# Performance work log

Hardware: AMD Instinct MI355X
Metric: run time of the kernel (lower is better)

Reference implementation:

```python
import jax, jax.numpy as jnp
import numpy as np

N_CAM = 6; C = 256; K = 100; GK = 200; NUM_CLASSES = 10; PROB_BIN = 64
SHAPES = [(72, 128), (36, 64), (18, 32)]
H_PAD, W_PAD = 576.0, 1024.0


def _make_anchors(shapes, grid_size=0.05, eps=0.01):
    parts = []
    for lvl, (h, w) in enumerate(shapes):
        gy, gx = jnp.meshgrid(jnp.arange(h, dtype=jnp.float32), jnp.arange(w, dtype=jnp.float32), indexing='ij')
        xy = (jnp.stack([gx, gy], -1) + 0.5) / jnp.array([w, h], jnp.float32)
        wh = jnp.full_like(xy, grid_size * 2.0 ** lvl)
        parts.append(jnp.concatenate([xy, wh], -1).reshape(-1, 4))
    a = jnp.concatenate(parts, 0)[None]  # [1, L, 4]
    valid = jnp.all((a > eps) & (a < 1 - eps), -1, keepdims=True)
    a = jnp.where(valid, jnp.log(a / (1 - a)), jnp.inf)
    return a, valid


def _layernorm(x, g, b, eps=1e-5):
    m = jnp.mean(x, -1, keepdims=True)
    v = jnp.var(x, -1, keepdims=True)
    return (x - m) * jax.lax.rsqrt(v + eps) * g + b


def _center2lidar(c2d, depths, intr, ext_inv):
    # c2d: [NK,2], depths: [NK,D], intr/ext_inv: [NK,4,4]
    fx = jnp.clip(intr[:, 0, 0], 1e-6)[:, None]
    fy = jnp.clip(intr[:, 1, 1], 1e-6)[:, None]
    cx = intr[:, 0, 2][:, None]; cy = intr[:, 1, 2][:, None]
    X = (c2d[:, 0:1] - cx) / fx * depths
    Y = (c2d[:, 1:2] - cy) / fy * depths
    pts = jnp.stack([X, Y, depths, jnp.ones_like(depths)], -1)  # [NK, D, 4]
    return jnp.einsum('ndk,njk->ndj', pts, ext_inv)[..., :3]


def setup_inputs():
    key = jax.random.key(0)
    ks = iter(jax.random.split(key, 48))
    def feat(shape):
        return jax.random.normal(next(ks), shape, dtype=jnp.float32)
    def w(shape):
        return (jax.random.normal(next(ks), shape) * 0.02).astype(jnp.float32)
    inp = {}
    for i, (h, wdt) in enumerate(SHAPES):
        inp[f'feat{i}'] = feat((N_CAM, C, h, wdt))
    rng = np.random.default_rng(0)
    Km = np.tile(np.eye(4, dtype=np.float32), (N_CAM, 1, 1))
    Km[:, 0, 0] = 500.0 + 10.0 * rng.standard_normal(N_CAM)
    Km[:, 1, 1] = 500.0 + 10.0 * rng.standard_normal(N_CAM)
    Km[:, 0, 2] = 512.0; Km[:, 1, 2] = 288.0
    E = np.tile(np.eye(4, dtype=np.float32), (N_CAM, 1, 1))
    for i in range(N_CAM):
        th = 2.0 * np.pi * i / N_CAM
        E[i, :3, :3] = np.array([[np.cos(th), -np.sin(th), 0.0], [np.sin(th), np.cos(th), 0.0], [0.0, 0.0, 1.0]], np.float32)
        E[i, :3, 3] = rng.standard_normal(3).astype(np.float32)
    inp['intrinsics'] = jnp.asarray(Km)[None]
    inp['extrinsics'] = jnp.asarray(E)[None]
    inp['extrinsics_inv'] = jnp.asarray(np.linalg.inv(E).astype(np.float32))[None]
    inp['w_proj0'] = w((C, C)); inp['w_proj1'] = w((C, C)); inp['w_proj2'] = w((C, C))
    inp['w_enc'] = w((C, C)); inp['b_enc'] = jnp.zeros((C,), jnp.float32)
    inp['ln_g'] = jnp.ones((C,), jnp.float32); inp['ln_b'] = jnp.zeros((C,), jnp.float32)
    inp['w_cls'] = w((C, NUM_CLASSES)); inp['b_cls'] = jnp.zeros((NUM_CLASSES,), jnp.float32)
    inp['w_bb1'] = w((C, C)); inp['b_bb1'] = jnp.zeros((C,), jnp.float32)
    inp['w_bb2'] = w((C, C)); inp['b_bb2'] = jnp.zeros((C,), jnp.float32)
    inp['w_bb3'] = w((C, 4)); inp['b_bb3'] = jnp.zeros((4,), jnp.float32)
    inp['depth_bins'] = jnp.linspace(1.0, 60.0, PROB_BIN, dtype=jnp.float32)
    inp['w_d1'] = w((C + 16, C)); inp['b_d1'] = jnp.zeros((C,), jnp.float32)
    inp['w_d2'] = w((C, PROB_BIN)); inp['b_d2'] = jnp.zeros((PROB_BIN,), jnp.float32)
    inp['w_m1'] = w((14, C)); inp['b_m1'] = jnp.zeros((C,), jnp.float32)
    inp['w_mg'] = w((C, C)); inp['b_mg'] = jnp.ones((C,), jnp.float32)
    inp['w_mb'] = w((C, C)); inp['b_mb'] = jnp.zeros((C,), jnp.float32)
    return inp


def reference(feat0, feat1, feat2, intrinsics, extrinsics, extrinsics_inv,
              w_proj0, w_proj1, w_proj2, w_enc, b_enc, ln_g, ln_b,
              w_cls, b_cls, w_bb1, b_bb1, w_bb2, b_bb2, w_bb3, b_bb3,
              depth_bins, w_d1, b_d1, w_d2, b_d2,
              w_m1, b_m1, w_mg, b_mg, w_mb, b_mb):
    intr = intrinsics[0]; ext = extrinsics[0]; ext_inv = extrinsics_inv[0]
    feats = [feat0, feat1, feat2]
    projs = [w_proj0, w_proj1, w_proj2]
    # flatten to [N_cam, HW, C] and apply 1x1 input projection
    tok = [jnp.einsum('nchw,cd->nhwd', f, wp).reshape(N_CAM, -1, C) for f, wp in zip(feats, projs)]
    memory = jnp.concatenate(tok, axis=1)  # [N_cam, L, C]
    anchors, valid = _make_anchors(SHAPES)
    out_mem = _layernorm((memory * valid.astype(memory.dtype)) @ w_enc + b_enc, ln_g, ln_b)
    enc_cls = out_mem @ w_cls + b_cls
    h = jax.nn.relu(out_mem @ w_bb1 + b_bb1)
    h = jax.nn.relu(h @ w_bb2 + b_bb2)
    enc_bbox = h @ w_bb3 + b_bb3 + anchors
    topk_scores, topk_ind = jax.lax.top_k(jnp.max(enc_cls, -1), K)  # [N_cam, K]
    query_feats = jnp.take_along_axis(out_mem, topk_ind[..., None], axis=1)  # [N_cam, K, C]
    ref_boxes = jax.nn.sigmoid(jnp.take_along_axis(enc_bbox, topk_ind[..., None], axis=1))  # [N_cam, K, 4]
    NK = N_CAM * K
    intr_q = jnp.broadcast_to(intr[:, None], (N_CAM, K, 4, 4)).reshape(NK, 4, 4)
    ext_inv_q = jnp.broadcast_to(ext_inv[:, None], (N_CAM, K, 4, 4)).reshape(NK, 4, 4)
    qf_flat = jax.lax.stop_gradient(query_feats).reshape(NK, C)
    depth_in = jnp.concatenate([qf_flat, intr_q.reshape(NK, 16) * 0.01], -1)
    dl = jax.nn.relu(depth_in @ w_d1 + b_d1) @ w_d2 + b_d2
    dl = jnp.nan_to_num(dl, nan=0.0, posinf=1e4, neginf=-1e4)
    depth_prob = jax.nn.softmax(dl.astype(jnp.float32), -1)  # [NK, D]
    c2d = jnp.stack([ref_boxes[..., 0].reshape(-1) * W_PAD, ref_boxes[..., 1].reshape(-1) * H_PAD], -1)
    depths = jnp.broadcast_to(depth_bins[None], (NK, PROB_BIN))
    center = _center2lidar(c2d, depths, intr_q, ext_inv_q)  # [NK, D, 3]
    dyn_query = jnp.concatenate([center, depth_prob[..., None]], -1)  # [NK, D, 4]
    _, gidx = jax.lax.top_k(topk_scores.reshape(-1), GK)
    dyn_query = dyn_query[gidx]
    qf_out = qf_flat[gidx]
    # MLN spatial alignment over raw encoder levels 0..1
    intr_s = intr / 1000.0
    mln_in = jnp.concatenate([intr_s[:, 0, 0:1], intr_s[:, 1, 1:2], ext[:, :3, :].reshape(N_CAM, 12)], -1)[:, None]  # [N,1,14]
    ff = jnp.concatenate([feat0.reshape(N_CAM, C, -1).transpose(0, 2, 1),
                          feat1.reshape(N_CAM, C, -1).transpose(0, 2, 1)], 1)  # [N, L_img, C]
    hm = jax.nn.relu(mln_in @ w_m1 + b_m1)
    gamma = hm @ w_mg + b_mg
    beta = hm @ w_mb + b_mb
    feat_flatten = ff * gamma + beta
    spatial_flatten = jnp.array([[s[0], s[1]] for s in SHAPES[:2]], jnp.int32)
    lidar2img = jnp.einsum('nij,njk->nik', intr, ext)[None]
    return (feat_flatten, spatial_flatten, lidar2img, dyn_query[None], qf_out[None])
```

## Files before the change

### kernel.cpp

```cpp
#include <hip/hip_runtime.h>
#include <math.h>

#define DEVI __device__ __forceinline__

constexpr int CAMS = 6;
constexpr int CH   = 256;
constexpr int LTOT = 12096;
constexpr int TPC  = 189;
constexpr int LIMG = 11520;

constexpr size_t WS_OM = 0;
constexpr size_t WS_SC = WS_OM + (size_t)CAMS*LTOT*CH;
constexpr size_t WS_TI = WS_SC + (size_t)CAMS*LTOT;
constexpr size_t WS_TS = WS_TI + 768;
constexpr size_t WS_DA = WS_TS + 768;
constexpr size_t WS_GI = WS_DA + (size_t)600*256;
constexpr size_t WS_GS = WS_GI + 256;
constexpr size_t WS_GA = WS_GS + 256;
constexpr size_t WS_BE = WS_GA + 1536;
constexpr size_t WS_AI = WS_BE + 1536;
constexpr size_t WS_AS = WS_AI + 3712;

constexpr size_t O_FF  = 0;
constexpr size_t O_SP  = (size_t)CAMS*LIMG*CH;
constexpr size_t O_L2I = O_SP + 4;
constexpr size_t O_DQ  = O_L2I + 96;
constexpr size_t O_QF  = O_DQ + (size_t)200*64*4;

DEVI float anchor_comp(int l, int j) {
    int W, wsh, ll; float Wf, Hf;
    if (l < 9216)      { W=128; wsh=7; Wf=128.f; Hf=72.f; ll=l; }
    else if (l < 11520){ W=64;  wsh=6; Wf=64.f;  Hf=36.f; ll=l-9216; }
    else               { W=32;  wsh=5; Wf=32.f;  Hf=18.f; ll=l-11520; }
    int y = ll >> wsh, x = ll & (W-1);
    float px = (x + 0.5f) / Wf;
    float py = (y + 0.5f) / Hf;
    bool valid = (px > 0.01f) && (px < 0.99f) && (py > 0.01f) && (py < 0.99f);
    if (!valid) return INFINITY;
    float p = (j == 0) ? px : py;
    return logf(p / (1.f - p));
}

__global__ __launch_bounds__(256, 3)
void k_proj(const float* __restrict__ f0, const float* __restrict__ f1, const float* __restrict__ f2,
            const float* __restrict__ wp0, const float* __restrict__ wp1, const float* __restrict__ wp2,
            float* __restrict__ Mout)
{
    __shared__ __align__(16) float lds[2*2048 + 2*512];
    float* wbufs = lds;
    float* abufs = lds + 4096;

    const int bx = blockIdx.x;
    const int n  = bx / TPC;
    const int l0 = (bx % TPC) * 64;
    const float* feat; const float* wp;
    int HW, lloc, W, wsh; float Wf, Hf;
    if (l0 < 9216)      { feat=f0; wp=wp0; HW=9216; lloc=l0;       W=128; wsh=7; Wf=128.f; Hf=72.f; }
    else if (l0 < 11520){ feat=f1; wp=wp1; HW=2304; lloc=l0-9216;  W=64;  wsh=6; Wf=64.f;  Hf=36.f; }
    else                { feat=f2; wp=wp2; HW=576;  lloc=l0-11520; W=32;  wsh=5; Wf=32.f;  Hf=18.f; }
    const float* featn = feat + (size_t)n*CH*HW;

    const int tid  = threadIdx.x;
    const int rg   = tid >> 5;
    const int cg   = tid & 31;
    const int sc_  = tid >> 5;
    const int sg   = tid & 31;
    const int arow = tid >> 4;
    const int ag   = tid & 15;

    float4 wreg0, wreg1;
    float4 areg;

    auto loadW = [&](int ck) {
        const float* p = wp + (size_t)(ck*8 + sc_)*256 + sg*8;
        wreg0 = *reinterpret_cast<const float4*>(p);
        wreg1 = *reinterpret_cast<const float4*>(p + 4);
    };
    auto writeW = [&](int b) {
        float* d = wbufs + b*2048 + sc_*256;
        *reinterpret_cast<float4*>(d + sg*4)       = wreg0;
        *reinterpret_cast<float4*>(d + 128 + sg*4) = wreg1;
    };
    auto loadA = [&](int ck) {
        if (tid < 128)
            areg = *reinterpret_cast<const float4*>(featn + (size_t)(ck*8 + arow)*HW + lloc + ag*4);
    };
    auto writeA = [&](int b) {
        if (tid < 128)
            *reinterpret_cast<float4*>(abufs + b*512 + arow*64 + ag*4) = areg;
    };

    float acc[8][8];
    #pragma unroll
    for (int r=0;r<8;++r)
        #pragma unroll
        for (int j=0;j<8;++j) acc[r][j] = 0.f;

    loadW(0); loadA(0);
    writeW(0); writeA(0);
    __syncthreads();
    int buf = 0;
    for (int k = 0; k < 32; ++k) {
        if (k < 31) { loadW(k+1); loadA(k+1); }
        const float* wb = wbufs + buf*2048;
        const float* ab = abufs + buf*512;
        #pragma unroll 2
        for (int c = 0; c < 8; ++c) {
            float4 a0 = *reinterpret_cast<const float4*>(ab + c*64 + rg*8);
            float4 a1 = *reinterpret_cast<const float4*>(ab + c*64 + rg*8 + 4);
            float4 w0 = *reinterpret_cast<const float4*>(wb + c*256 + cg*4);
            float4 w1 = *reinterpret_cast<const float4*>(wb + c*256 + 128 + cg*4);
            float av[8] = {a0.x,a0.y,a0.z,a0.w, a1.x,a1.y,a1.z,a1.w};
            float wv[8] = {w0.x,w0.y,w0.z,w0.w, w1.x,w1.y,w1.z,w1.w};
            #pragma unroll
            for (int r=0;r<8;++r)
                #pragma unroll
                for (int j=0;j<8;++j)
                    acc[r][j] = fmaf(av[r], wv[j], acc[r][j]);
        }
        if (k < 31) { writeW(buf^1); writeA(buf^1); }
        __syncthreads();
        buf ^= 1;
    }

    #pragma unroll
    for (int r=0;r<8;++r) {
        int ll = lloc + rg*8 + r;
        int y = ll >> wsh, x = ll & (W-1);
        float px = (x + 0.5f) / Wf;
        float py = (y + 0.5f) / Hf;
        bool valid = (px > 0.01f) && (px < 0.99f) && (py > 0.01f) && (py < 0.99f);
        float m = valid ? 1.f : 0.f;
        float* dst = Mout + ((size_t)n*LTOT + l0 + rg*8 + r)*CH + cg*8;
        *reinterpret_cast<float4*>(dst)   = make_float4(acc[r][0]*m,acc[r][1]*m,acc[r][2]*m,acc[r][3]*m);
        *reinterpret_cast<float4*>(dst+4) = make_float4(acc[r][4]*m,acc[r][5]*m,acc[r][6]*m,acc[r][7]*m);
    }
}

__global__ __launch_bounds__(256, 3)
void k_enc(float* __restrict__ M,
           const float* __restrict__ w_enc, const float* __restrict__ b_enc,
           const float* __restrict__ ln_g, const float* __restrict__ ln_b,
           const float* __restrict__ w_cls, const float* __restrict__ b_cls,
           float* __restrict__ scores)
{
    __shared__ __align__(16) float lds[2*2048 + 2*512];
    float* wbufs = lds;
    float* abufs = lds + 4096;

    const int bx = blockIdx.x;
    const int n  = bx / TPC;
    const int l0 = (bx % TPC) * 64;

    const int tid  = threadIdx.x;
    const int rg   = tid >> 5;
    const int cg   = tid & 31;
    const int sc_  = tid >> 5;
    const int sg   = tid & 31;
    const int tok  = tid & 63;
    const int cq   = (tid >> 6) & 1;

    float4 wreg0, wreg1;
    float4 mreg;

    auto loadW = [&](int ck) {
        const float* p = w_enc + (size_t)(ck*8 + sc_)*256 + sg*8;
        wreg0 = *reinterpret_cast<const float4*>(p);
        wreg1 = *reinterpret_cast<const float4*>(p + 4);
    };
    auto writeW = [&](int b) {
        float* d = wbufs + b*2048 + sc_*256;
        *reinterpret_cast<float4*>(d + sg*4)       = wreg0;
        *reinterpret_cast<float4*>(d + 128 + sg*4) = wreg1;
    };
    auto loadA = [&](int ck) {
        if (tid < 128)
            mreg = *reinterpret_cast<const float4*>(M + ((size_t)n*LTOT + l0 + tok)*CH + ck*8 + cq*4);
    };
    auto writeA = [&](int b) {
        if (tid < 128) {
            float* d = abufs + b*512 + tok;
            d[(cq*4+0)*64] = mreg.x;
            d[(cq*4+1)*64] = mreg.y;
            d[(cq*4+2)*64] = mreg.z;
            d[(cq*4+3)*64] = mreg.w;
        }
    };

    float acc[8][8];
    #pragma unroll
    for (int r=0;r<8;++r)
        #pragma unroll
        for (int j=0;j<8;++j) acc[r][j] = 0.f;

    loadW(0); loadA(0);
    writeW(0); writeA(0);
    __syncthreads();
    int buf = 0;
    for (int k = 0; k < 32; ++k) {
        if (k < 31) { loadW(k+1); loadA(k+1); }
        const float* wb = wbufs + buf*2048;
        const float* ab = abufs + buf*512;
        #pragma unroll 2
        for (int c = 0; c < 8; ++c) {
            float4 a0 = *reinterpret_cast<const float4*>(ab + c*64 + rg*8);
            float4 a1 = *reinterpret_cast<const float4*>(ab + c*64 + rg*8 + 4);
            float4 w0 = *reinterpret_cast<const float4*>(wb + c*256 + cg*4);
            float4 w1 = *reinterpret_cast<const float4*>(wb + c*256 + 128 + cg*4);
            float av[8] = {a0.x,a0.y,a0.z,a0.w, a1.x,a1.y,a1.z,a1.w};
            float wv[8] = {w0.x,w0.y,w0.z,w0.w, w1.x,w1.y,w1.z,w1.w};
            #pragma unroll
            for (int r=0;r<8;++r)
                #pragma unroll
                for (int j=0;j<8;++j)
                    acc[r][j] = fmaf(av[r], wv[j], acc[r][j]);
        }
        if (k < 31) { writeW(buf^1); writeA(buf^1); }
        __syncthreads();
        buf ^= 1;
    }

    {
        float4 be0 = *reinterpret_cast<const float4*>(b_enc + cg*8);
        float4 be1 = *reinterpret_cast<const float4*>(b_enc + cg*8 + 4);
        float4 g0  = *reinterpret_cast<const float4*>(ln_g  + cg*8);
        float4 g1  = *reinterpret_cast<const float4*>(ln_g  + cg*8 + 4);
        float4 bb0 = *reinterpret_cast<const float4*>(ln_b  + cg*8);
        float4 bb1 = *reinterpret_cast<const float4*>(ln_b  + cg*8 + 4);
        float bev[8] = {be0.x,be0.y,be0.z,be0.w, be1.x,be1.y,be1.z,be1.w};
        float gv[8]  = {g0.x,g0.y,g0.z,g0.w, g1.x,g1.y,g1.z,g1.w};
        float bv[8]  = {bb0.x,bb0.y,bb0.z,bb0.w, bb1.x,bb1.y,bb1.z,bb1.w};
        #pragma unroll
        for (int r=0;r<8;++r) {
            float s = 0.f;
            #pragma unroll
            for (int j=0;j<8;++j) { acc[r][j] += bev[j]; s += acc[r][j]; }
            s += __shfl_xor(s,1); s += __shfl_xor(s,2); s += __shfl_xor(s,4);
            s += __shfl_xor(s,8); s += __shfl_xor(s,16);
            float mean = s * (1.f/256.f);
            float vs = 0.f;
            #pragma unroll
            for (int j=0;j<8;++j) { float d = acc[r][j]-mean; vs = fmaf(d,d,vs); }
            vs += __shfl_xor(vs,1); vs += __shfl_xor(vs,2); vs += __shfl_xor(vs,4);
            vs += __shfl_xor(vs,8); vs += __shfl_xor(vs,16);
            float rs = 1.f / sqrtf(vs*(1.f/256.f) + 1e-5f);
            #pragma unroll
            for (int j=0;j<8;++j) acc[r][j] = (acc[r][j]-mean)*rs*gv[j] + bv[j];
        }
    }

    #pragma unroll
    for (int r=0;r<8;++r) {
        float* dst = M + ((size_t)n*LTOT + l0 + rg*8 + r)*CH + cg*8;
        *reinterpret_cast<float4*>(dst)   = make_float4(acc[r][0],acc[r][1],acc[r][2],acc[r][3]);
        *reinterpret_cast<float4*>(dst+4) = make_float4(acc[r][4],acc[r][5],acc[r][6],acc[r][7]);
    }

    {
        float bcl[10];
        #pragma unroll
        for (int c=0;c<10;++c) bcl[c] = b_cls[c];
        #pragma unroll
        for (int r=0;r<8;++r) {
            float p[10];
            #pragma unroll
            for (int c=0;c<10;++c) p[c] = 0.f;
            #pragma unroll
            for (int i=0;i<8;++i) {
                const float* wc = w_cls + (cg*8+i)*10;
                float a = acc[r][i];
                #pragma unroll
                for (int c=0;c<10;c+=2) {
                    float2 w2 = *reinterpret_cast<const float2*>(wc + c);
                    p[c]   = fmaf(a, w2.x, p[c]);
                    p[c+1] = fmaf(a, w2.y, p[c+1]);
                }
            }
            #pragma unroll
            for (int c=0;c<10;++c) {
                p[c] += __shfl_xor(p[c],1); p[c] += __shfl_xor(p[c],2);
                p[c] += __shfl_xor(p[c],4); p[c] += __shfl_xor(p[c],8);
                p[c] += __shfl_xor(p[c],16);
            }
            if (cg == 0) {
                float mx = -INFINITY;
                #pragma unroll
                for (int c=0;c<10;++c) mx = fmaxf(mx, p[c] + bcl[c]);
                scores[(size_t)n*LTOT + l0 + rg*8 + r] = mx;
            }
        }
    }
}

typedef unsigned long long u64;

DEVI u64 pack_key(float s, unsigned idx) {
    unsigned u = __float_as_uint(s);
    u = (u & 0x80000000u) ? ~u : (u | 0x80000000u);
    return ((u64)u << 32) | (unsigned)(~idx);
}
DEVI float key_score(u64 k) {
    unsigned u = (unsigned)(k >> 32);
    u = (u & 0x80000000u) ? (u ^ 0x80000000u) : ~u;
    return __uint_as_float(u);
}
DEVI int key_idx(u64 k) { return (int)(~(unsigned)k); }

template<int N>
DEVI void bitonic_desc(u64* s, int tid) {
    for (int size = 2; size <= N; size <<= 1) {
        for (int stride = size >> 1; stride > 0; stride >>= 1) {
            __syncthreads();
            #pragma unroll 2
            for (int t = tid; t < N/2; t += 256) {
                int lo = ((t & ~(stride-1)) << 1) | (t & (stride-1));
                int hi = lo + stride;
                bool desc = ((lo & size) == 0);
                u64 a = s[lo], b = s[hi];
                if ((a < b) == desc) { s[lo] = b; s[hi] = a; }
            }
        }
    }
    __syncthreads();
}

__global__ __launch_bounds__(256)
void k_sortA(const float* __restrict__ scores, int* __restrict__ outi, float* __restrict__ outs)
{
    __shared__ u64 s[2048];
    const int b = blockIdx.x, tid = threadIdx.x;
    const int cam = b / 6, seg = b % 6;
    const float* v = scores + (size_t)cam*LTOT + seg*2016;
    for (int i = tid; i < 2048; i += 256)
        s[i] = (i < 2016) ? pack_key(v[i], seg*2016 + i) : 0ull;
    bitonic_desc<2048>(s, tid);
    if (tid < 100) {
        u64 k = s[tid];
        outi[b*100 + tid] = key_idx(k);
        outs[b*100 + tid] = key_score(k);
    }
}

__global__ __launch_bounds__(256)
void k_sortB(const int* __restrict__ ai, const float* __restrict__ as,
             int* __restrict__ ti, float* __restrict__ ts)
{
    __shared__ u64 s[1024];
    const int cam = blockIdx.x, tid = threadIdx.x;
    for (int i = tid; i < 1024; i += 256)
        s[i] = (i < 600) ? pack_key(as[cam*600 + i], (unsigned)ai[cam*600 + i]) : 0ull;
    bitonic_desc<1024>(s, tid);
    if (tid < 100) {
        u64 k = s[tid];
        ti[cam*100 + tid] = key_idx(k);
        ts[cam*100 + tid] = key_score(k);
    }
}

__global__ __launch_bounds__(256)
void k_sortC(const float* __restrict__ ts, int* __restrict__ gi)
{
    __shared__ u64 s[1024];
    const int tid = threadIdx.x;
    for (int i = tid; i < 1024; i += 256)
        s[i] = (i < 600) ? pack_key(ts[i], (unsigned)i) : 0ull;
    bitonic_desc<1024>(s, tid);
    if (tid < 200) gi[tid] = key_idx(s[tid]);
}

__global__ __launch_bounds__(256)
void k_query(const float* __restrict__ out_mem, const int* __restrict__ topk_ind,
             const float* __restrict__ intr, const float* __restrict__ ext_inv,
             const float* __restrict__ w_bb1, const float* __restrict__ b_bb1,
             const float* __restrict__ w_bb2, const float* __restrict__ b_bb2,
             const float* __restrict__ w_bb3, const float* __restrict__ b_bb3,
             const float* __restrict__ depth_bins,
             const float* __restrict__ w_d1, const float* __restrict__ b_d1,
             const float* __restrict__ w_d2, const float* __restrict__ b_d2,
             float* __restrict__ dyn_all)
{
    __shared__ float sq[272];
    __shared__ float sh[256];
    __shared__ float sh2[256];
    __shared__ float sbb[2];
    const int nk = blockIdx.x;
    const int n = nk / 100;
    const int tid = threadIdx.x;
    const int l = topk_ind[nk];
    sq[tid] = out_mem[((size_t)n*LTOT + l)*CH + tid];
    if (tid < 16) sq[256+tid] = intr[n*16+tid] * 0.01f;
    __syncthreads();
    float s1 = b_bb1[tid];
    for (int c=0;c<256;++c) s1 = fmaf(sq[c], w_bb1[c*256+tid], s1);
    sh[tid] = fmaxf(s1, 0.f);
    __syncthreads();
    float s2 = b_bb2[tid];
    for (int c=0;c<256;++c) s2 = fmaf(sh[c], w_bb2[c*256+tid], s2);
    sh2[tid] = fmaxf(s2, 0.f);
    __syncthreads();
    {
        int j = tid >> 6, c0 = tid & 63;
        if (j < 2) {
            float p = 0.f;
            #pragma unroll
            for (int t=0;t<4;++t) { int c = c0 + t*64; p = fmaf(sh2[c], w_bb3[c*4+j], p); }
            #pragma unroll
            for (int m=1;m<64;m<<=1) p += __shfl_xor(p, m);
            if (c0 == 0) sbb[j] = p + b_bb3[j] + anchor_comp(l, j);
        }
    }
    float t1 = b_d1[tid];
    for (int c=0;c<272;++c) t1 = fmaf(sq[c], w_d1[c*256+tid], t1);
    sh[tid] = fmaxf(t1, 0.f);
    __syncthreads();
    if (tid < 64) {
        float dl = b_d2[tid];
        for (int c=0;c<256;++c) dl = fmaf(sh[c], w_d2[c*64+tid], dl);
        if (isnan(dl)) dl = 0.f;
        if (isinf(dl)) dl = (dl > 0.f) ? 1e4f : -1e4f;
        float mx = dl;
        #pragma unroll
        for (int m=1;m<64;m<<=1) mx = fmaxf(mx, __shfl_xor(mx, m));
        float e = expf(dl - mx);
        float sum = e;
        #pragma unroll
        for (int m=1;m<64;m<<=1) sum += __shfl_xor(sum, m);
        float dp = e / sum;
        float fx = fmaxf(intr[n*16+0], 1e-6f);
        float fy = fmaxf(intr[n*16+5], 1e-6f);
        float cx = intr[n*16+2], cy = intr[n*16+6];
        float sx = 1.f/(1.f+expf(-sbb[0]));
        float sy = 1.f/(1.f+expf(-sbb[1]));
        float c2dx = sx * 1024.f, c2dy = sy * 576.f;
        float dep = depth_bins[tid];
        float X = (c2dx - cx)/fx*dep;
        float Y = (c2dy - cy)/fy*dep;
        const float* EI = ext_inv + n*16;
        float c0v = EI[0]*X + EI[1]*Y + EI[2]*dep + EI[3];
        float c1v = EI[4]*X + EI[5]*Y + EI[6]*dep + EI[7];
        float c2v = EI[8]*X + EI[9]*Y + EI[10]*dep + EI[11];
        float4 o = make_float4(c0v, c1v, c2v, dp);
        *reinterpret_cast<float4*>(dyn_all + ((size_t)nk*64 + tid)*4) = o;
    }
}

__global__ __launch_bounds__(256)
void k_gather(const float* __restrict__ dyn_all, const int* __restrict__ gidx,
              const int* __restrict__ topk_ind, const float* __restrict__ out_mem,
              float* __restrict__ out)
{
    int g = blockIdx.x, tid = threadIdx.x;
    int src = gidx[g];
    out[O_DQ + (size_t)g*256 + tid] = dyn_all[(size_t)src*256 + tid];
    int n = src/100; int l = topk_ind[src];
    out[O_QF + (size_t)g*256 + tid] = out_mem[((size_t)n*LTOT + l)*CH + tid];
}

__global__ __launch_bounds__(256)
void k_mln(const float* __restrict__ intr, const float* __restrict__ ext,
           const float* __restrict__ w_m1, const float* __restrict__ b_m1,
           const float* __restrict__ w_mg, const float* __restrict__ b_mg,
           const float* __restrict__ w_mb, const float* __restrict__ b_mb,
           float* __restrict__ gamma, float* __restrict__ beta)
{
    __shared__ float hm[256];
    int tid = threadIdx.x;
    for (int n=0;n<CAMS;++n) {
        float m[14];
        m[0] = intr[n*16+0] / 1000.0f;
        m[1] = intr[n*16+5] / 1000.0f;
        #pragma unroll
        for (int j=0;j<12;++j) m[2+j] = ext[n*16+j];
        float h = b_m1[tid];
        #pragma unroll
        for (int k=0;k<14;++k) h = fmaf(m[k], w_m1[k*256+tid], h);
        hm[tid] = fmaxf(h, 0.f);
        __syncthreads();
        float g = b_mg[tid], bt = b_mb[tid];
        for (int c=0;c<256;++c) {
            float hv = hm[c];
            g  = fmaf(hv, w_mg[c*256+tid], g);
            bt = fmaf(hv, w_mb[c*256+tid], bt);
        }
        gamma[n*256+tid] = g;
        beta[n*256+tid]  = bt;
        __syncthreads();
    }
}

__global__ __launch_bounds__(256)
void k_flatten(const float* __restrict__ f0, const float* __restrict__ f1,
               const float* __restrict__ gamma, const float* __restrict__ beta,
               float* __restrict__ out)
{
    __shared__ float t[64][65];
    int b = blockIdx.x;
    int lt = b % 180, ct = (b/180) & 3, n = b / 720;
    int l0 = lt*64, c0 = ct*64;
    const float* f; int HW, lb;
    if (l0 < 9216) { f=f0; HW=9216; lb=l0; } else { f=f1; HW=2304; lb=l0-9216; }
    int tid = threadIdx.x;
    int cl = tid >> 4, lw = (tid & 15)*4;
    #pragma unroll
    for (int rep=0;rep<4;++rep) {
        int cc = cl + rep*16;
        float4 v = *reinterpret_cast<const float4*>(f + ((size_t)n*CH + c0+cc)*HW + lb + lw);
        t[cc][lw+0]=v.x; t[cc][lw+1]=v.y; t[cc][lw+2]=v.z; t[cc][lw+3]=v.w;
    }
    __syncthreads();
    int ll = tid >> 4, cw = (tid & 15)*4;
    float4 gv = *reinterpret_cast<const float4*>(gamma + n*256 + c0 + cw);
    float4 bv = *reinterpret_cast<const float4*>(beta  + n*256 + c0 + cw);
    #pragma unroll
    for (int rep=0;rep<4;++rep) {
        int l = ll + rep*16;
        float4 o;
        o.x = fmaf(t[cw+0][l], gv.x, bv.x);
        o.y = fmaf(t[cw+1][l], gv.y, bv.y);
        o.z = fmaf(t[cw+2][l], gv.z, bv.z);
        o.w = fmaf(t[cw+3][l], gv.w, bv.w);
        *reinterpret_cast<float4*>(out + ((size_t)n*LIMG + l0 + l)*CH + c0 + cw) = o;
    }
}

__global__ void k_small(const float* __restrict__ intr, const float* __restrict__ ext,
                        float* __restrict__ out)
{
    int tid = threadIdx.x;
    if (tid < 4) {
        const float sp[4] = {72.f, 128.f, 36.f, 64.f};
        out[O_SP + tid] = sp[tid];
    }
    if (tid < 96) {
        int n = tid >> 4, i = (tid >> 2) & 3, k = tid & 3;
        float s = 0.f;
        #pragma unroll
        for (int j=0;j<4;++j) s = fmaf(intr[n*16 + i*4 + j], ext[n*16 + j*4 + k], s);
        out[O_L2I + tid] = s;
    }
}

extern "C" void kernel_launch(void* const* d_in, const int* in_sizes, int n_in,
                              void* d_out, int out_size, void* d_ws, size_t ws_size,
                              hipStream_t stream) {
    const float* f0      = (const float*)d_in[0];
    const float* f1      = (const float*)d_in[1];
    const float* f2      = (const float*)d_in[2];
    const float* intr    = (const float*)d_in[3];
    const float* ext     = (const float*)d_in[4];
    const float* ext_inv = (const float*)d_in[5];
    const float* wp0     = (const float*)d_in[6];
    const float* wp1     = (const float*)d_in[7];
    const float* wp2     = (const float*)d_in[8];
    const float* w_enc   = (const float*)d_in[9];
    const float* b_enc   = (const float*)d_in[10];
    const float* ln_g    = (const float*)d_in[11];
    const float* ln_b    = (const float*)d_in[12];
    const float* w_cls   = (const float*)d_in[13];
    const float* b_cls   = (const float*)d_in[14];
    const float* w_bb1   = (const float*)d_in[15];
    const float* b_bb1   = (const float*)d_in[16];
    const float* w_bb2   = (const float*)d_in[17];
    const float* b_bb2   = (const float*)d_in[18];
    const float* w_bb3   = (const float*)d_in[19];
    const float* b_bb3   = (const float*)d_in[20];
    const float* dbins   = (const float*)d_in[21];
    const float* w_d1    = (const float*)d_in[22];
    const float* b_d1    = (const float*)d_in[23];
    const float* w_d2    = (const float*)d_in[24];
    const float* b_d2    = (const float*)d_in[25];
    const float* w_m1    = (const float*)d_in[26];
    const float* b_m1    = (const float*)d_in[27];
    const float* w_mg    = (const float*)d_in[28];
    const float* b_mg    = (const float*)d_in[29];
    const float* w_mb    = (const float*)d_in[30];
    const float* b_mb    = (const float*)d_in[31];

    float* ws  = (float*)d_ws;
    float* out = (float*)d_out;
    float* om  = ws + WS_OM;
    float* sc  = ws + WS_SC;
    int*   ti  = (int*)(ws + WS_TI);
    float* ts  = ws + WS_TS;
    float* da  = ws + WS_DA;
    int*   gi  = (int*)(ws + WS_GI);
    float* ga  = ws + WS_GA;
    float* be  = ws + WS_BE;
    int*   ai  = (int*)(ws + WS_AI);
    float* as  = ws + WS_AS;

    k_proj<<<CAMS*TPC, 256, 0, stream>>>(f0, f1, f2, wp0, wp1, wp2, om);
    k_enc<<<CAMS*TPC, 256, 0, stream>>>(om, w_enc, b_enc, ln_g, ln_b, w_cls, b_cls, sc);
    k_sortA<<<36, 256, 0, stream>>>(sc, ai, as);
    k_sortB<<<6, 256, 0, stream>>>(ai, as, ti, ts);
    k_query<<<600, 256, 0, stream>>>(om, ti, intr, ext_inv,
                                     w_bb1, b_bb1, w_bb2, b_bb2, w_bb3, b_bb3,
                                     dbins, w_d1, b_d1, w_d2, b_d2, da);
    k_sortC<<<1, 256, 0, stream>>>(ts, gi);
    k_gather<<<200, 256, 0, stream>>>(da, gi, ti, om, out);
    k_mln<<<1, 256, 0, stream>>>(intr, ext, w_m1, b_m1, w_mg, b_mg, w_mb, b_mb, ga, be);
    k_flatten<<<6*4*180, 256, 0, stream>>>(f0, f1, ga, be, out);
    k_small<<<1, 128, 0, stream>>>(intr, ext, out);
}
```

Baseline: 456.8 us.

## Double token tile per block in projection and encoder GEMM kernels

Both GEMM-style kernels now process 128 tokens per block instead of 64, so each thread holds a 16x8 accumulator instead of 8x8. All 256 threads now stage the activation tile, and the last, partial tile is handled with clamped loads and guarded stores. The aim is higher arithmetic intensity and fewer redundant weight loads per output. The cost is much higher register pressure: launch bounds drop to one block per CU and the grid roughly halves, which may hurt latency hiding and load balance.

```diff
diff --git a/kernel.cpp b/kernel.cpp
--- a/kernel.cpp
+++ b/kernel.cpp
@@ -6,7 +6,7 @@
 constexpr int CAMS = 6;
 constexpr int CH   = 256;
 constexpr int LTOT = 12096;
-constexpr int TPC  = 189;
+constexpr int TPC2 = 95;
 constexpr int LIMG = 11520;
 
 constexpr size_t WS_OM = 0;
@@ -41,18 +41,18 @@
     return logf(p / (1.f - p));
 }
 
-__global__ __launch_bounds__(256, 3)
+__global__ __launch_bounds__(256, 1)
 void k_proj(const float* __restrict__ f0, const float* __restrict__ f1, const float* __restrict__ f2,
             const float* __restrict__ wp0, const float* __restrict__ wp1, const float* __restrict__ wp2,
             float* __restrict__ Mout)
 {
-    __shared__ __align__(16) float lds[2*2048 + 2*512];
+    __shared__ __align__(16) float lds[2*2048 + 2*1024];
     float* wbufs = lds;
     float* abufs = lds + 4096;
 
     const int bx = blockIdx.x;
-    const int n  = bx / TPC;
-    const int l0 = (bx % TPC) * 64;
+    const int n  = bx / TPC2;
+    const int l0 = (bx % TPC2) * 128;
     const float* feat; const float* wp;
     int HW, lloc, W, wsh; float Wf, Hf;
     if (l0 < 9216)      { feat=f0; wp=wp0; HW=9216; lloc=l0;       W=128; wsh=7; Wf=128.f; Hf=72.f; }
@@ -60,16 +60,15 @@
     else                { feat=f2; wp=wp2; HW=576;  lloc=l0-11520; W=32;  wsh=5; Wf=32.f;  Hf=18.f; }
     const float* featn = feat + (size_t)n*CH*HW;
 
-    const int tid  = threadIdx.x;
-    const int rg   = tid >> 5;
-    const int cg   = tid & 31;
-    const int sc_  = tid >> 5;
-    const int sg   = tid & 31;
-    const int arow = tid >> 4;
-    const int ag   = tid & 15;
-
-    float4 wreg0, wreg1;
-    float4 areg;
+    const int tid = threadIdx.x;
+    const int rg  = tid >> 5;
+    const int cg  = tid & 31;
+    const int sc_ = tid >> 5;
+    const int sg  = tid & 31;
+    const int ac  = tid >> 5;
+    const int at4 = (tid & 31) * 4;
+
+    float4 wreg0, wreg1, areg;
 
     auto loadW = [&](int ck) {
         const float* p = wp + (size_t)(ck*8 + sc_)*256 + sg*8;
@@ -82,17 +81,17 @@
         *reinterpret_cast<float4*>(d + 128 + sg*4) = wreg1;
     };
     auto loadA = [&](int ck) {
-        if (tid < 128)
-            areg = *reinterpret_cast<const float4*>(featn + (size_t)(ck*8 + arow)*HW + lloc + ag*4);
+        int off = lloc + at4;
+        if (off > HW - 4) off = HW - 4;
+        areg = *reinterpret_cast<const float4*>(featn + (size_t)(ck*8 + ac)*HW + off);
     };
     auto writeA = [&](int b) {
-        if (tid < 128)
-            *reinterpret_cast<float4*>(abufs + b*512 + arow*64 + ag*4) = areg;
-    };
-
-    float acc[8][8];
+        *reinterpret_cast<float4*>(abufs + b*1024 + tid*4) = areg;
+    };
+
+    float acc[16][8];
     #pragma unroll
-    for (int r=0;r<8;++r)
+    for (int r=0;r<16;++r)
         #pragma unroll
         for (int j=0;j<8;++j) acc[r][j] = 0.f;
 
@@ -103,17 +102,20 @@
     for (int k = 0; k < 32; ++k) {
         if (k < 31) { loadW(k+1); loadA(k+1); }
         const float* wb = wbufs + buf*2048;
-        const float* ab = abufs + buf*512;
-        #pragma unroll 2
+        const float* ab = abufs + buf*1024;
+        #pragma unroll 1
         for (int c = 0; c < 8; ++c) {
-            float4 a0 = *reinterpret_cast<const float4*>(ab + c*64 + rg*8);
-            float4 a1 = *reinterpret_cast<const float4*>(ab + c*64 + rg*8 + 4);
+            float4 a0 = *reinterpret_cast<const float4*>(ab + c*128 + rg*16);
+            float4 a1 = *reinterpret_cast<const float4*>(ab + c*128 + rg*16 + 4);
+            float4 a2 = *reinterpret_cast<const float4*>(ab + c*128 + rg*16 + 8);
+            float4 a3 = *reinterpret_cast<const float4*>(ab + c*128 + rg*16 + 12);
             float4 w0 = *reinterpret_cast<const float4*>(wb + c*256 + cg*4);
             float4 w1 = *reinterpret_cast<const float4*>(wb + c*256 + 128 + cg*4);
-            float av[8] = {a0.x,a0.y,a0.z,a0.w, a1.x,a1.y,a1.z,a1.w};
-            float wv[8] = {w0.x,w0.y,w0.z,w0.w, w1.x,w1.y,w1.z,w1.w};
-            #pragma unroll
-            for (int r=0;r<8;++r)
+            float av[16] = {a0.x,a0.y,a0.z,a0.w, a1.x,a1.y,a1.z,a1.w,
+                            a2.x,a2.y,a2.z,a2.w, a3.x,a3.y,a3.z,a3.w};
+            float wv[8]  = {w0.x,w0.y,w0.z,w0.w, w1.x,w1.y,w1.z,w1.w};
+            #pragma unroll
+            for (int r=0;r<16;++r)
                 #pragma unroll
                 for (int j=0;j<8;++j)
                     acc[r][j] = fmaf(av[r], wv[j], acc[r][j]);
@@ -124,44 +126,45 @@
     }
 
     #pragma unroll
-    for (int r=0;r<8;++r) {
-        int ll = lloc + rg*8 + r;
+    for (int r=0;r<16;++r) {
+        int glob = l0 + rg*16 + r;
+        if (glob >= LTOT) continue;
+        int ll = lloc + rg*16 + r;
         int y = ll >> wsh, x = ll & (W-1);
         float px = (x + 0.5f) / Wf;
         float py = (y + 0.5f) / Hf;
         bool valid = (px > 0.01f) && (px < 0.99f) && (py > 0.01f) && (py < 0.99f);
         float m = valid ? 1.f : 0.f;
-        float* dst = Mout + ((size_t)n*LTOT + l0 + rg*8 + r)*CH + cg*8;
+        float* dst = Mout + ((size_t)n*LTOT + glob)*CH + cg*8;
         *reinterpret_cast<float4*>(dst)   = make_float4(acc[r][0]*m,acc[r][1]*m,acc[r][2]*m,acc[r][3]*m);
         *reinterpret_cast<float4*>(dst+4) = make_float4(acc[r][4]*m,acc[r][5]*m,acc[r][6]*m,acc[r][7]*m);
     }
 }
 
-__global__ __launch_bounds__(256, 3)
+__global__ __launch_bounds__(256, 1)
 void k_enc(float* __restrict__ M,
            const float* __restrict__ w_enc, const float* __restrict__ b_enc,
            const float* __restrict__ ln_g, const float* __restrict__ ln_b,
            const float* __restrict__ w_cls, const float* __restrict__ b_cls,
            float* __restrict__ scores)
 {
-    __shared__ __align__(16) float lds[2*2048 + 2*512];
+    __shared__ __align__(16) float lds[2*2048 + 2*1024];
     float* wbufs = lds;
     float* abufs = lds + 4096;
 
     const int bx = blockIdx.x;
-    const int n  = bx / TPC;
-    const int l0 = (bx % TPC) * 64;
-
-    const int tid  = threadIdx.x;
-    const int rg   = tid >> 5;
-    const int cg   = tid & 31;
-    const int sc_  = tid >> 5;
-    const int sg   = tid & 31;
-    const int tok  = tid & 63;
-    const int cq   = (tid >> 6) & 1;
-
-    float4 wreg0, wreg1;
-    float4 mreg;
+    const int n  = bx / TPC2;
+    const int l0 = (bx % TPC2) * 128;
+
+    const int tid = threadIdx.x;
+    const int rg  = tid >> 5;
+    const int cg  = tid & 31;
+    const int sc_ = tid >> 5;
+    const int sg  = tid & 31;
+    const int tok = tid & 127;
+    const int cp  = (tid >> 7) * 4;
+
+    float4 wreg0, wreg1, mreg;
 
     auto loadW = [&](int ck) {
         const float* p = w_enc + (size_t)(ck*8 + sc_)*256 + sg*8;
@@ -174,22 +177,19 @@
         *reinterpret_cast<float4*>(d + 128 + sg*4) = wreg1;
     };
     auto loadA = [&](int ck) {
-        if (tid < 128)
-            mreg = *reinterpret_cast<const float4*>(M + ((size_t)n*LTOT + l0 + tok)*CH + ck*8 + cq*4);
+        mreg = *reinterpret_cast<const float4*>(M + ((size_t)n*LTOT + l0 + tok)*CH + ck*8 + cp);
     };
     auto writeA = [&](int b) {
-        if (tid < 128) {
-            float* d = abufs + b*512 + tok;
-            d[(cq*4+0)*64] = mreg.x;
-            d[(cq*4+1)*64] = mreg.y;
-            d[(cq*4+2)*64] = mreg.z;
-            d[(cq*4+3)*64] = mreg.w;
-        }
-    };
-
-    float acc[8][8];
+        float* d = abufs + b*1024 + tok;
+        d[(cp+0)*128] = mreg.x;
+        d[(cp+1)*128] = mreg.y;
+        d[(cp+2)*128] = mreg.z;
+        d[(cp+3)*128] = mreg.w;
+    };
+
+    float acc[16][8];
     #pragma unroll
-    for (int r=0;r<8;++r)
+    for (int r=0;r<16;++r)
         #pragma unroll
         for (int j=0;j<8;++j) acc[r][j] = 0.f;
 
@@ -200,17 +200,20 @@
     for (int k = 0; k < 32; ++k) {
         if (k < 31) { loadW(k+1); loadA(k+1); }
         const float* wb = wbufs + buf*2048;
-        const float* ab = abufs + buf*512;
-        #pragma unroll 2
+        const float* ab = abufs + buf*1024;
+        #pragma unroll 1
         for (int c = 0; c < 8; ++c) {
-            float4 a0 = *reinterpret_cast<const float4*>(ab + c*64 + rg*8);
-            float4 a1 = *reinterpret_cast<const float4*>(ab + c*64 + rg*8 + 4);
+            float4 a0 = *reinterpret_cast<const float4*>(ab + c*128 + rg*16);
+            float4 a1 = *reinterpret_cast<const float4*>(ab + c*128 + rg*16 + 4);
+            float4 a2 = *reinterpret_cast<const float4*>(ab + c*128 + rg*16 + 8);
+            float4 a3 = *reinterpret_cast<const float4*>(ab + c*128 + rg*16 + 12);
             float4 w0 = *reinterpret_cast<const float4*>(wb + c*256 + cg*4);
             float4 w1 = *reinterpret_cast<const float4*>(wb + c*256 + 128 + cg*4);
-            float av[8] = {a0.x,a0.y,a0.z,a0.w, a1.x,a1.y,a1.z,a1.w};
-            float wv[8] = {w0.x,w0.y,w0.z,w0.w, w1.x,w1.y,w1.z,w1.w};
-            #pragma unroll
-            for (int r=0;r<8;++r)
+            float av[16] = {a0.x,a0.y,a0.z,a0.w, a1.x,a1.y,a1.z,a1.w,
+                            a2.x,a2.y,a2.z,a2.w, a3.x,a3.y,a3.z,a3.w};
+            float wv[8]  = {w0.x,w0.y,w0.z,w0.w, w1.x,w1.y,w1.z,w1.w};
+            #pragma unroll
+            for (int r=0;r<16;++r)
                 #pragma unroll
                 for (int j=0;j<8;++j)
                     acc[r][j] = fmaf(av[r], wv[j], acc[r][j]);
@@ -231,7 +234,7 @@
         float gv[8]  = {g0.x,g0.y,g0.z,g0.w, g1.x,g1.y,g1.z,g1.w};
         float bv[8]  = {bb0.x,bb0.y,bb0.z,bb0.w, bb1.x,bb1.y,bb1.z,bb1.w};
         #pragma unroll
-        for (int r=0;r<8;++r) {
+        for (int r=0;r<16;++r) {
             float s = 0.f;
             #pragma unroll
             for (int j=0;j<8;++j) { acc[r][j] += bev[j]; s += acc[r][j]; }
@@ -249,19 +252,18 @@
         }
     }
 
-    #pragma unroll
-    for (int r=0;r<8;++r) {
-        float* dst = M + ((size_t)n*LTOT + l0 + rg*8 + r)*CH + cg*8;
-        *reinterpret_cast<float4*>(dst)   = make_float4(acc[r][0],acc[r][1],acc[r][2],acc[r][3]);
-        *reinterpret_cast<float4*>(dst+4) = make_float4(acc[r][4],acc[r][5],acc[r][6],acc[r][7]);
-    }
-
     {
         float bcl[10];
         #pragma unroll
         for (int c=0;c<10;++c) bcl[c] = b_cls[c];
         #pragma unroll
-        for (int r=0;r<8;++r) {
+        for (int r=0;r<16;++r) {
+            int glob = l0 + rg*16 + r;
+            if (glob < LTOT) {
+                float* dst = M + ((size_t)n*LTOT + glob)*CH + cg*8;
+                *reinterpret_cast<float4*>(dst)   = make_float4(acc[r][0],acc[r][1],acc[r][2],acc[r][3]);
+                *reinterpret_cast<float4*>(dst+4) = make_float4(acc[r][4],acc[r][5],acc[r][6],acc[r][7]);
+            }
             float p[10];
             #pragma unroll
             for (int c=0;c<10;++c) p[c] = 0.f;
@@ -282,11 +284,11 @@
                 p[c] += __shfl_xor(p[c],4); p[c] += __shfl_xor(p[c],8);
                 p[c] += __shfl_xor(p[c],16);
             }
-            if (cg == 0) {
+            if (cg == 0 && glob < LTOT) {
                 float mx = -INFINITY;
                 #pragma unroll
                 for (int c=0;c<10;++c) mx = fmaxf(mx, p[c] + bcl[c]);
-                scores[(size_t)n*LTOT + l0 + rg*8 + r] = mx;
+                scores[(size_t)n*LTOT + glob] = mx;
             }
         }
     }
@@ -589,8 +591,8 @@
     int*   ai  = (int*)(ws + WS_AI);
     float* as  = ws + WS_AS;
 
-    k_proj<<<CAMS*TPC, 256, 0, stream>>>(f0, f1, f2, wp0, wp1, wp2, om);
-    k_enc<<<CAMS*TPC, 256, 0, stream>>>(om, w_enc, b_enc, ln_g, ln_b, w_cls, b_cls, sc);
+    k_proj<<<CAMS*TPC2, 256, 0, stream>>>(f0, f1, f2, wp0, wp1, wp2, om);
+    k_enc<<<CAMS*TPC2, 256, 0, stream>>>(om, w_enc, b_enc, ln_g, ln_b, w_cls, b_cls, sc);
     k_sortA<<<36, 256, 0, stream>>>(sc, ai, as);
     k_sortB<<<6, 256, 0, stream>>>(ai, as, ti, ts);
     k_query<<<600, 256, 0, stream>>>(om, ti, intr, ext_inv,
```

Measured after the change: 566.0 us. 1.24x slower.
